# Performance work log

Measured on AMD Instinct MI355X. Metric: run time of the kernel, lower is better.

Reference implementation:

```python
import jax, jax.numpy as jnp
import numpy as np

SEQ_LEN, BATCH, INPUT_SIZE, HIDDEN_SIZE = 2048, 512, 64, 128


def setup_inputs() -> dict:
    key = jax.random.key(0)
    kx, k1, kb1, k2, kb2 = jax.random.split(key, 5)
    s1 = 1.0 / np.sqrt(INPUT_SIZE)
    s2 = 1.0 / np.sqrt(HIDDEN_SIZE)
    return {
        "x": jax.random.normal(kx, (SEQ_LEN, BATCH, INPUT_SIZE), dtype=jnp.float32),
        "W1": jax.random.uniform(k1, (HIDDEN_SIZE, INPUT_SIZE), jnp.float32, -s1, s1),
        "b1": jax.random.uniform(kb1, (HIDDEN_SIZE,), jnp.float32, -s1, s1),
        "W2": jax.random.uniform(k2, (HIDDEN_SIZE, HIDDEN_SIZE), jnp.float32, -s2, s2),
        "b2": jax.random.uniform(kb2, (HIDDEN_SIZE,), jnp.float32, -s2, s2),
    }


def reference(x, W1, b1, W2, b2):
    # Elman RNN: h_t = tanh(fc2(h_{t-1}) + fc1(x_t)), h_0 = 0
    # x: (S, B, I); W1: (H, I); W2: (H, H)
    B = x.shape[1]
    H = W2.shape[0]
    h0 = jnp.zeros((B, H), dtype=x.dtype)

    def step(h, x_t):
        h_new = jnp.tanh(x_t @ W1.T + b1 + h @ W2.T + b2)
        return h_new, h_new

    h_last, h_seq = jax.lax.scan(step, h0, x)
    return h_seq, h_last[None]  # (S,B,H), (1,B,H)
```

## Files before the change

### kernel.cpp

```cpp
#include <hip/hip_runtime.h>
#include <math.h>


#define S_LEN 2048
#define B_SZ  512
#define I_SZ  64
#define H_SZ  128
#define BT    16
#define BLK   512
#define HROW  256
#define XROW  128

typedef short bf16x8 __attribute__((ext_vector_type(8)));
typedef float f32x4  __attribute__((ext_vector_type(4)));

#define MFMA(A, B, C) __builtin_amdgcn_mfma_f32_16x16x32_bf16((A), (B), (C), 0, 0, 0)

#define LDS_BARRIER()                                        \
    asm volatile("s_waitcnt lgkmcnt(0)" ::: "memory");       \
    __builtin_amdgcn_s_barrier();                            \
    asm volatile("" ::: "memory")

__device__ __forceinline__ unsigned short bf_trunc(float v) {
    union { float f; unsigned u; } x; x.f = v;
    return (unsigned short)(x.u >> 16);
}
__device__ __forceinline__ float bf_to_f(unsigned short h) {
    union { float f; unsigned u; } x; x.u = ((unsigned)h) << 16;
    return x.f;
}

__global__ __launch_bounds__(BLK) void rnn_mfma(
    const float* __restrict__ x,
    const float* __restrict__ W1,
    const float* __restrict__ b1,
    const float* __restrict__ W2,
    const float* __restrict__ b2,
    float* __restrict__ out)
{
    const int tid  = threadIdx.x;
    const int lane = tid & 63;
    const int w    = tid >> 6;
    const int l15  = lane & 15;
    const int l4   = lane >> 4;
    const int unit = (w << 4) + l15;
    const int b0   = blockIdx.x * BT;

    __shared__ short hpl_hi[2][BT * H_SZ];
    __shared__ short hpl_lo[2][BT * H_SZ];
    __shared__ short xpl_hi[2][BT * I_SZ];
    __shared__ short xpl_lo[2][BT * I_SZ];

    bf16x8 w2h[4], w2l[4], w1h[2], w1l[2];
    #pragma unroll
    for (int c = 0; c < 4; ++c) {
        #pragma unroll
        for (int j = 0; j < 8; ++j) {
            float v = W2[unit * H_SZ + 32 * c + l4 * 8 + j];
            unsigned short hi = bf_trunc(v);
            unsigned short lo = bf_trunc(v - bf_to_f(hi));
            w2h[c][j] = (short)hi; w2l[c][j] = (short)lo;
        }
    }
    #pragma unroll
    for (int c = 0; c < 2; ++c) {
        #pragma unroll
        for (int j = 0; j < 8; ++j) {
            float v = W1[unit * I_SZ + 32 * c + l4 * 8 + j];
            unsigned short hi = bf_trunc(v);
            unsigned short lo = bf_trunc(v - bf_to_f(hi));
            w1h[c][j] = (short)hi; w1l[c][j] = (short)lo;
        }
    }
    const float zb = b1[unit] + b2[unit];

    int hro[4], xro[2], woh[4];
    #pragma unroll
    for (int c = 0; c < 4; ++c)
        hro[c] = l15 * HROW + ((64 * c + l4 * 16) ^ ((l15 & 7) << 4));
    #pragma unroll
    for (int c = 0; c < 2; ++c)
        xro[c] = l15 * XROW + ((64 * c + l4 * 16) ^ ((l15 & 7) << 4));
    #pragma unroll
    for (int r = 0; r < 4; ++r) {
        int row = (l4 << 2) + r;
        woh[r] = row * HROW + ((unit * 2) ^ ((row & 7) << 4));
    }
    const int xr  = tid >> 5;
    const int xc  = (tid & 31) * 2;
    const int wox = xr * XROW + ((xc * 2) ^ ((xr & 7) << 4));

    {
        float2 v0 = *(const float2*)(x + ((size_t)0 * B_SZ + b0 + xr) * I_SZ + xc);
        unsigned short h0 = bf_trunc(v0.x), h1 = bf_trunc(v0.y);
        unsigned short g0 = bf_trunc(v0.x - bf_to_f(h0));
        unsigned short g1 = bf_trunc(v0.y - bf_to_f(h1));
        *(unsigned*)((char*)xpl_hi[0] + wox) = (unsigned)h0 | ((unsigned)h1 << 16);
        *(unsigned*)((char*)xpl_lo[0] + wox) = (unsigned)g0 | ((unsigned)g1 << 16);
    }
    float2 xgA = *(const float2*)(x + ((size_t)1 * B_SZ + b0 + xr) * I_SZ + xc);
    float2 xgB;

    LDS_BARRIER();

    bf16x8 ah[4], al[4], xh[2], xl[2];
    #pragma unroll
    for (int c = 0; c < 4; ++c) { ah[c] = (bf16x8){0,0,0,0,0,0,0,0}; al[c] = ah[c]; }
    #pragma unroll
    for (int c = 0; c < 2; ++c) {
        xh[c] = *(const bf16x8*)((const char*)xpl_hi[0] + xro[c]);
        xl[c] = *(const bf16x8*)((const char*)xpl_lo[0] + xro[c]);
    }

#define STEP(S, XGC, XGL, HB)                                                 \
{                                                                             \
                 \
    { int sp = (S) + 2; if (sp > S_LEN - 1) sp = S_LEN - 1;                   \
      XGL = *(const float2*)(x + ((size_t)sp * B_SZ + b0 + xr) * I_SZ + xc); }\
    f32x4 accA = {zb, zb, zb, zb};                                            \
    f32x4 accB = {0.f, 0.f, 0.f, 0.f};                                       \
    f32x4 accC = {0.f, 0.f, 0.f, 0.f};                                       \
    accA = MFMA(ah[0], w2h[0], accA);  accB = MFMA(al[0], w2h[0], accB);      \
    accC = MFMA(ah[0], w2l[0], accC);                                         \
    accA = MFMA(ah[1], w2h[1], accA);  accB = MFMA(al[1], w2h[1], accB);      \
    accC = MFMA(ah[1], w2l[1], accC);                                         \
    accA = MFMA(ah[2], w2h[2], accA);  accB = MFMA(al[2], w2h[2], accB);      \
    accC = MFMA(ah[2], w2l[2], accC);                                         \
    accA = MFMA(ah[3], w2h[3], accA);  accB = MFMA(al[3], w2h[3], accB);      \
    accC = MFMA(ah[3], w2l[3], accC);                                         \
    accA = MFMA(xh[0], w1h[0], accA);  accB = MFMA(xl[0], w1h[0], accB);      \
    accC = MFMA(xh[0], w1l[0], accC);                                         \
    accA = MFMA(xh[1], w1h[1], accA);  accB = MFMA(xl[1], w1h[1], accB);      \
    accC = MFMA(xh[1], w1l[1], accC);                                         \
    f32x4 acc = (accA + accB) + accC;                                         \
                      \
    _Pragma("unroll")                                                         \
    for (int r = 0; r < 4; ++r) {                                             \
        float a = acc[r];                                                     \
        float t = 1.0f - 2.0f * __builtin_amdgcn_rcpf(1.0f + __expf(2.0f*a)); \
        int row = (l4 << 2) + r;                                              \
        out[((size_t)(S) * B_SZ + b0 + row) * H_SZ + unit] = t;               \
        unsigned short hi = bf_trunc(t);                                      \
        unsigned short lo = bf_trunc(t - bf_to_f(hi));                        \
        *(short*)((char*)hpl_hi[HB] + woh[r]) = (short)hi;                    \
        *(short*)((char*)hpl_lo[HB] + woh[r]) = (short)lo;                    \
    }                                                                         \
                        \
    {                                                                         \
        unsigned short h0 = bf_trunc(XGC.x), h1 = bf_trunc(XGC.y);            \
        unsigned short g0 = bf_trunc(XGC.x - bf_to_f(h0));                    \
        unsigned short g1 = bf_trunc(XGC.y - bf_to_f(h1));                    \
        *(unsigned*)((char*)xpl_hi[HB] + wox) = (unsigned)h0|((unsigned)h1<<16);\
        *(unsigned*)((char*)xpl_lo[HB] + wox) = (unsigned)g0|((unsigned)g1<<16);\
    }                                                                         \
    LDS_BARRIER();                                                            \
                                                \
    _Pragma("unroll")                                                         \
    for (int c = 0; c < 4; ++c) {                                             \
        ah[c] = *(const bf16x8*)((const char*)hpl_hi[HB] + hro[c]);           \
        al[c] = *(const bf16x8*)((const char*)hpl_lo[HB] + hro[c]);           \
    }                                                                         \
    _Pragma("unroll")                                                         \
    for (int c = 0; c < 2; ++c) {                                             \
        xh[c] = *(const bf16x8*)((const char*)xpl_hi[HB] + xro[c]);           \
        xl[c] = *(const bf16x8*)((const char*)xpl_lo[HB] + xro[c]);           \
    }                                                                         \
}

    for (int s2 = 0; s2 < S_LEN; s2 += 2) {
        STEP(s2,     xgA, xgB, 1);
        STEP(s2 + 1, xgB, xgA, 0);
    }
#undef STEP

    #pragma unroll
    for (int r = 0; r < 4; ++r) {
        int row = (l4 << 2) + r;
        unsigned short hi = (unsigned short)*(short*)((char*)hpl_hi[0] + woh[r]);
        unsigned short lo = (unsigned short)*(short*)((char*)hpl_lo[0] + woh[r]);
        float hv = bf_to_f(hi) + bf_to_f(lo);
        out[(size_t)S_LEN * B_SZ * H_SZ + (size_t)(b0 + row) * H_SZ + unit] = hv;
    }
}

extern "C" void kernel_launch(void* const* d_in, const int* in_sizes, int n_in,
                              void* d_out, int out_size, void* d_ws, size_t ws_size,
                              hipStream_t stream) {
    const float* x  = (const float*)d_in[0];
    const float* W1 = (const float*)d_in[1];
    const float* b1 = (const float*)d_in[2];
    const float* W2 = (const float*)d_in[3];
    const float* b2 = (const float*)d_in[4];
    float* out = (float*)d_out;

    rnn_mfma<<<dim3(B_SZ / BT), dim3(BLK), 0, stream>>>(x, W1, b1, W2, b2, out);
}
```

Before: 1.297 ms.

## Hoist input projection into parallel prepass and shrink recurrent block to two waves

Splits the work into a fully parallel prepass that computes x·W1ᵀ+b1+b2 for all timesteps into the output buffer, and a recurrent kernel that only does the h·W2ᵀ MFMAs. The recurrent block drops from 8 waves to 2, with each wave handling 64 hidden units, and the hidden state is stored as fp32 in LDS and split into hi/lo on read. This takes the input MFMAs and x conversion off the serial critical path and means fewer waves per barrier. The cost is an extra full-size write and read of the precomputed terms, and the final h_last is now the fp32 value rather than the hi+lo sum.

New measurement: 2.879 ms. 122% more time.

```diff
diff --git a/kernel.cpp b/kernel.cpp
--- a/kernel.cpp
+++ b/kernel.cpp
@@ -7,9 +7,10 @@
 #define I_SZ  64
 #define H_SZ  128
 #define BT    16
-#define BLK   512
-#define HROW  256
-#define XROW  128
+#define NTILE 32
+#define BLK1  512
+#define BLK2  128
+#define SBH   (B_SZ * H_SZ)
 
 typedef short bf16x8 __attribute__((ext_vector_type(8)));
 typedef float f32x4  __attribute__((ext_vector_type(4)));
@@ -21,21 +22,73 @@
     __builtin_amdgcn_s_barrier();                            \
     asm volatile("" ::: "memory")
 
+__device__ __forceinline__ unsigned fbits(float v) {
+    union { float f; unsigned u; } x; x.f = v; return x.u;
+}
+__device__ __forceinline__ float fval(unsigned u) {
+    union { float f; unsigned u; } x; x.u = u; return x.f;
+}
+__device__ __forceinline__ unsigned short bf_rnd(float v) {
+    return (unsigned short)((fbits(v) + 0x8000u) >> 16);
+}
 __device__ __forceinline__ unsigned short bf_trunc(float v) {
-    union { float f; unsigned u; } x; x.f = v;
-    return (unsigned short)(x.u >> 16);
-}
-__device__ __forceinline__ float bf_to_f(unsigned short h) {
-    union { float f; unsigned u; } x; x.u = ((unsigned)h) << 16;
-    return x.f;
-}
-
-__global__ __launch_bounds__(BLK) void rnn_mfma(
+    return (unsigned short)(fbits(v) >> 16);
+}
+__device__ __forceinline__ void split8t(float4 a, float4 b, bf16x8* hi, bf16x8* lo) {
+    float v[8] = {a.x, a.y, a.z, a.w, b.x, b.y, b.z, b.w};
+    #pragma unroll
+    for (int j = 0; j < 8; ++j) {
+        unsigned short h = bf_trunc(v[j]);
+        (*hi)[j] = (short)h;
+        (*lo)[j] = (short)bf_trunc(v[j] - fval(((unsigned)h) << 16));
+    }
+}
+
+__global__ __launch_bounds__(BLK1) void rnn_prepass(
     const float* __restrict__ x,
     const float* __restrict__ W1,
     const float* __restrict__ b1,
+    const float* __restrict__ b2,
+    float* __restrict__ z)
+{
+    const int tid  = threadIdx.x;
+    const int lane = tid & 63;
+    const int w    = tid >> 6;
+    const int l15  = lane & 15;
+    const int l4   = lane >> 4;
+    const int unit = (w << 4) + l15;
+    const int bid  = blockIdx.x;
+    const int s    = bid >> 5;
+    const int b0   = (bid & 31) << 4;
+
+    bf16x8 w1h[2], w1l[2];
+    #pragma unroll
+    for (int c = 0; c < 2; ++c) {
+        const float* wr = W1 + unit * I_SZ + 32 * c + l4 * 8;
+        split8t(*(const float4*)wr, *(const float4*)(wr + 4), &w1h[c], &w1l[c]);
+    }
+    const float zb = b1[unit] + b2[unit];
+
+    bf16x8 xh[2], xl[2];
+    const float* xr = x + ((size_t)s * B_SZ + b0 + l15) * I_SZ + l4 * 8;
+    #pragma unroll
+    for (int c = 0; c < 2; ++c)
+        split8t(*(const float4*)(xr + 32 * c), *(const float4*)(xr + 32 * c + 4),
+                &xh[c], &xl[c]);
+
+    f32x4 acc  = {zb, zb, zb, zb};
+    f32x4 acc2 = {0.f, 0.f, 0.f, 0.f};
+    acc  = MFMA(xh[0], w1h[0], acc);   acc  = MFMA(xh[1], w1h[1], acc);
+    acc2 = MFMA(xl[0], w1h[0], acc2);  acc2 = MFMA(xl[1], w1h[1], acc2);
+    acc2 = MFMA(xh[0], w1l[0], acc2);  acc2 = MFMA(xh[1], w1l[1], acc2);
+    acc += acc2;
+
+    *(f32x4*)(z + ((size_t)bid * 8 + w) * 256 + lane * 4) = acc;
+}
+
+__global__ __launch_bounds__(BLK2, 1) void rnn_recur(
     const float* __restrict__ W2,
-    const float* __restrict__ b2,
+    const float* __restrict__ zr,
     float* __restrict__ out)
 {
     const int tid  = threadIdx.x;
@@ -43,143 +96,129 @@
     const int w    = tid >> 6;
     const int l15  = lane & 15;
     const int l4   = lane >> 4;
-    const int unit = (w << 4) + l15;
-    const int b0   = blockIdx.x * BT;
-
-    __shared__ short hpl_hi[2][BT * H_SZ];
-    __shared__ short hpl_lo[2][BT * H_SZ];
-    __shared__ short xpl_hi[2][BT * I_SZ];
-    __shared__ short xpl_lo[2][BT * I_SZ];
-
-    bf16x8 w2h[4], w2l[4], w1h[2], w1l[2];
-    #pragma unroll
-    for (int c = 0; c < 4; ++c) {
-        #pragma unroll
-        for (int j = 0; j < 8; ++j) {
-            float v = W2[unit * H_SZ + 32 * c + l4 * 8 + j];
-            unsigned short hi = bf_trunc(v);
-            unsigned short lo = bf_trunc(v - bf_to_f(hi));
-            w2h[c][j] = (short)hi; w2l[c][j] = (short)lo;
+    const int tile = blockIdx.x;
+    const int b0   = tile << 4;
+
+    __shared__ float hplane[2][BT * H_SZ];
+
+    bf16x8 w2h[4][4], w2l[4][4];
+    #pragma unroll
+    for (int t = 0; t < 4; ++t) {
+        const int n = (w << 6) + (t << 4) + l15;
+        #pragma unroll
+        for (int c = 0; c < 4; ++c) {
+            const float* wr = W2 + n * H_SZ + 32 * c + l4 * 8;
+            split8t(*(const float4*)wr, *(const float4*)(wr + 4),
+                    &w2h[t][c], &w2l[t][c]);
         }
     }
-    #pragma unroll
-    for (int c = 0; c < 2; ++c) {
-        #pragma unroll
-        for (int j = 0; j < 8; ++j) {
-            float v = W1[unit * I_SZ + 32 * c + l4 * 8 + j];
-            unsigned short hi = bf_trunc(v);
-            unsigned short lo = bf_trunc(v - bf_to_f(hi));
-            w1h[c][j] = (short)hi; w1l[c][j] = (short)lo;
+
+    int rb[4][2];
+    #pragma unroll
+    for (int c = 0; c < 4; ++c)
+        #pragma unroll
+        for (int hh = 0; hh < 2; ++hh)
+            rb[c][hh] = l15 * 512 +
+                ((((32 * c + l4 * 8 + 4 * hh) << 2)) ^ ((l15 & 7) << 4));
+    int wb[4][4];
+    #pragma unroll
+    for (int t = 0; t < 4; ++t)
+        #pragma unroll
+        for (int r = 0; r < 4; ++r) {
+            int row = (l4 << 2) + r;
+            wb[t][r] = row * 512 +
+                ((((w << 6) + (t << 4) + l15) << 2) ^ ((row & 7) << 4));
         }
-    }
-    const float zb = b1[unit] + b2[unit];
-
-    int hro[4], xro[2], woh[4];
-    #pragma unroll
-    for (int c = 0; c < 4; ++c)
-        hro[c] = l15 * HROW + ((64 * c + l4 * 16) ^ ((l15 & 7) << 4));
-    #pragma unroll
-    for (int c = 0; c < 2; ++c)
-        xro[c] = l15 * XROW + ((64 * c + l4 * 16) ^ ((l15 & 7) << 4));
-    #pragma unroll
-    for (int r = 0; r < 4; ++r) {
-        int row = (l4 << 2) + r;
-        woh[r] = row * HROW + ((unit * 2) ^ ((row & 7) << 4));
-    }
-    const int xr  = tid >> 5;
-    const int xc  = (tid & 31) * 2;
-    const int wox = xr * XROW + ((xc * 2) ^ ((xr & 7) << 4));
+
+    const float* zp = zr + (size_t)tile * 2048 + (size_t)(4 * w) * 256 + lane * 4;
+    const size_t obase = (size_t)(b0 + (l4 << 2)) * H_SZ + (w << 6) + l15;
+
+    f32x4 zA[4], zB[4];
+    #pragma unroll
+    for (int t = 0; t < 4; ++t) {
+        zA[t] = *(const f32x4*)(zp + t * 256);
+        zB[t] = *(const f32x4*)(zp + t * 256 + SBH);
+    }
+    bf16x8 ah[4], al[4];
+    #pragma unroll
+    for (int c = 0; c < 4; ++c) { ah[c] = (bf16x8){0,0,0,0,0,0,0,0}; al[c] = ah[c]; }
+    float tl[4][4];
+    union U { unsigned u[4]; bf16x8 v; };
+
+#define BODY(S, P, ZQ)                                                        \
+{                                                                             \
+    f32x4 acc[4], a2[4], a3[4];                                               \
+    _Pragma("unroll")                                                         \
+    for (int t = 0; t < 4; ++t) {                                             \
+        acc[t] = ZQ[t];                                                       \
+        a2[t] = (f32x4){0.f,0.f,0.f,0.f};  a3[t] = a2[t];                     \
+    }                                                                         \
+                   \
+    { int sp = (S) + 2; if (sp > S_LEN - 1) sp = S_LEN - 1;                   \
+      const float* zs = zp + (size_t)sp * SBH;                                \
+      _Pragma("unroll")                                                       \
+      for (int t = 0; t < 4; ++t) ZQ[t] = *(const f32x4*)(zs + t * 256); }    \
+    _Pragma("unroll")                                                         \
+    for (int c = 0; c < 4; ++c) {                                             \
+        _Pragma("unroll")                                                     \
+        for (int t = 0; t < 4; ++t) {                                         \
+            acc[t] = MFMA(ah[c], w2h[t][c], acc[t]);                          \
+            a2[t]  = MFMA(al[c], w2h[t][c], a2[t]);                           \
+            a3[t]  = MFMA(ah[c], w2l[t][c], a3[t]);                           \
+        }                                                                     \
+    }                                                                         \
+    float* po = out + (size_t)(S) * SBH + obase;                              \
+    _Pragma("unroll")                                                         \
+    for (int t = 0; t < 4; ++t) {                                             \
+        _Pragma("unroll")                                                     \
+        for (int r = 0; r < 4; ++r) {                                         \
+            float a = (acc[t][r] + a2[t][r]) + a3[t][r];                      \
+            float tt = 1.0f - 2.0f * __builtin_amdgcn_rcpf(1.0f + __expf(2.0f*a)); \
+            tl[t][r] = tt;                                                    \
+            po[(size_t)r * H_SZ + t * 16] = tt;                               \
+            *(float*)((char*)hplane[P] + wb[t][r]) = tt;                      \
+        }                                                                     \
+    }                                                                         \
+    LDS_BARRIER();                                                            \
+              \
+    _Pragma("unroll")                                                         \
+    for (int c = 0; c < 4; ++c) {                                             \
+        uint4 d0 = *(const uint4*)((const char*)hplane[P] + rb[c][0]);        \
+        uint4 d1 = *(const uint4*)((const char*)hplane[P] + rb[c][1]);        \
+        U uh, ul;                                                             \
+        uh.u[0] = __builtin_amdgcn_perm(d0.y, d0.x, 0x07060302u);             \
+        uh.u[1] = __builtin_amdgcn_perm(d0.w, d0.z, 0x07060302u);             \
+        uh.u[2] = __builtin_amdgcn_perm(d1.y, d1.x, 0x07060302u);             \
+        uh.u[3] = __builtin_amdgcn_perm(d1.w, d1.z, 0x07060302u);             \
+        unsigned e0 = fbits(fval(d0.x) - fval(d0.x & 0xffff0000u));           \
+        unsigned e1 = fbits(fval(d0.y) - fval(d0.y & 0xffff0000u));           \
+        unsigned e2 = fbits(fval(d0.z) - fval(d0.z & 0xffff0000u));           \
+        unsigned e3 = fbits(fval(d0.w) - fval(d0.w & 0xffff0000u));           \
+        unsigned e4 = fbits(fval(d1.x) - fval(d1.x & 0xffff0000u));           \
+        unsigned e5 = fbits(fval(d1.y) - fval(d1.y & 0xffff0000u));           \
+        unsigned e6 = fbits(fval(d1.z) - fval(d1.z & 0xffff0000u));           \
+        unsigned e7 = fbits(fval(d1.w) - fval(d1.w & 0xffff0000u));           \
+        ul.u[0] = __builtin_amdgcn_perm(e1, e0, 0x07060302u);                 \
+        ul.u[1] = __builtin_amdgcn_perm(e3, e2, 0x07060302u);                 \
+        ul.u[2] = __builtin_amdgcn_perm(e5, e4, 0x07060302u);                 \
+        ul.u[3] = __builtin_amdgcn_perm(e7, e6, 0x07060302u);                 \
+        ah[c] = uh.v;  al[c] = ul.v;                                          \
+    }                                                                         \
+}
+
+    for (int s2 = 0; s2 < S_LEN; s2 += 2) {
+        BODY(s2,     0, zA);
+        BODY(s2 + 1, 1, zB);
+    }
+#undef BODY
 
     {
-        float2 v0 = *(const float2*)(x + ((size_t)0 * B_SZ + b0 + xr) * I_SZ + xc);
-        unsigned short h0 = bf_trunc(v0.x), h1 = bf_trunc(v0.y);
-        unsigned short g0 = bf_trunc(v0.x - bf_to_f(h0));
-        unsigned short g1 = bf_trunc(v0.y - bf_to_f(h1));
-        *(unsigned*)((char*)xpl_hi[0] + wox) = (unsigned)h0 | ((unsigned)h1 << 16);
-        *(unsigned*)((char*)xpl_lo[0] + wox) = (unsigned)g0 | ((unsigned)g1 << 16);
-    }
-    float2 xgA = *(const float2*)(x + ((size_t)1 * B_SZ + b0 + xr) * I_SZ + xc);
-    float2 xgB;
-
-    LDS_BARRIER();
-
-    bf16x8 ah[4], al[4], xh[2], xl[2];
-    #pragma unroll
-    for (int c = 0; c < 4; ++c) { ah[c] = (bf16x8){0,0,0,0,0,0,0,0}; al[c] = ah[c]; }
-    #pragma unroll
-    for (int c = 0; c < 2; ++c) {
-        xh[c] = *(const bf16x8*)((const char*)xpl_hi[0] + xro[c]);
-        xl[c] = *(const bf16x8*)((const char*)xpl_lo[0] + xro[c]);
-    }
-
-#define STEP(S, XGC, XGL, HB)                                                 \
-{                                                                             \
-                 \
-    { int sp = (S) + 2; if (sp > S_LEN - 1) sp = S_LEN - 1;                   \
-      XGL = *(const float2*)(x + ((size_t)sp * B_SZ + b0 + xr) * I_SZ + xc); }\
-    f32x4 accA = {zb, zb, zb, zb};                                            \
-    f32x4 accB = {0.f, 0.f, 0.f, 0.f};                                       \
-    f32x4 accC = {0.f, 0.f, 0.f, 0.f};                                       \
-    accA = MFMA(ah[0], w2h[0], accA);  accB = MFMA(al[0], w2h[0], accB);      \
-    accC = MFMA(ah[0], w2l[0], accC);                                         \
-    accA = MFMA(ah[1], w2h[1], accA);  accB = MFMA(al[1], w2h[1], accB);      \
-    accC = MFMA(ah[1], w2l[1], accC);                                         \
-    accA = MFMA(ah[2], w2h[2], accA);  accB = MFMA(al[2], w2h[2], accB);      \
-    accC = MFMA(ah[2], w2l[2], accC);                                         \
-    accA = MFMA(ah[3], w2h[3], accA);  accB = MFMA(al[3], w2h[3], accB);      \
-    accC = MFMA(ah[3], w2l[3], accC);                                         \
-    accA = MFMA(xh[0], w1h[0], accA);  accB = MFMA(xl[0], w1h[0], accB);      \
-    accC = MFMA(xh[0], w1l[0], accC);                                         \
-    accA = MFMA(xh[1], w1h[1], accA);  accB = MFMA(xl[1], w1h[1], accB);      \
-    accC = MFMA(xh[1], w1l[1], accC);                                         \
-    f32x4 acc = (accA + accB) + accC;                                         \
-                      \
-    _Pragma("unroll")                                                         \
-    for (int r = 0; r < 4; ++r) {                                             \
-        float a = acc[r];                                                     \
-        float t = 1.0f - 2.0f * __builtin_amdgcn_rcpf(1.0f + __expf(2.0f*a)); \
-        int row = (l4 << 2) + r;                                              \
-        out[((size_t)(S) * B_SZ + b0 + row) * H_SZ + unit] = t;               \
-        unsigned short hi = bf_trunc(t);                                      \
-        unsigned short lo = bf_trunc(t - bf_to_f(hi));                        \
-        *(short*)((char*)hpl_hi[HB] + woh[r]) = (short)hi;                    \
-        *(short*)((char*)hpl_lo[HB] + woh[r]) = (short)lo;                    \
-    }                                                                         \
-                        \
-    {                                                                         \
-        unsigned short h0 = bf_trunc(XGC.x), h1 = bf_trunc(XGC.y);            \
-        unsigned short g0 = bf_trunc(XGC.x - bf_to_f(h0));                    \
-        unsigned short g1 = bf_trunc(XGC.y - bf_to_f(h1));                    \
-        *(unsigned*)((char*)xpl_hi[HB] + wox) = (unsigned)h0|((unsigned)h1<<16);\
-        *(unsigned*)((char*)xpl_lo[HB] + wox) = (unsigned)g0|((unsigned)g1<<16);\
-    }                                                                         \
-    LDS_BARRIER();                                                            \
-                                                \
-    _Pragma("unroll")                                                         \
-    for (int c = 0; c < 4; ++c) {                                             \
-        ah[c] = *(const bf16x8*)((const char*)hpl_hi[HB] + hro[c]);           \
-        al[c] = *(const bf16x8*)((const char*)hpl_lo[HB] + hro[c]);           \
-    }                                                                         \
-    _Pragma("unroll")                                                         \
-    for (int c = 0; c < 2; ++c) {                                             \
-        xh[c] = *(const bf16x8*)((const char*)xpl_hi[HB] + xro[c]);           \
-        xl[c] = *(const bf16x8*)((const char*)xpl_lo[HB] + xro[c]);           \
-    }                                                                         \
-}
-
-    for (int s2 = 0; s2 < S_LEN; s2 += 2) {
-        STEP(s2,     xgA, xgB, 1);
-        STEP(s2 + 1, xgB, xgA, 0);
-    }
-#undef STEP
-
-    #pragma unroll
-    for (int r = 0; r < 4; ++r) {
-        int row = (l4 << 2) + r;
-        unsigned short hi = (unsigned short)*(short*)((char*)hpl_hi[0] + woh[r]);
-        unsigned short lo = (unsigned short)*(short*)((char*)hpl_lo[0] + woh[r]);
-        float hv = bf_to_f(hi) + bf_to_f(lo);
-        out[(size_t)S_LEN * B_SZ * H_SZ + (size_t)(b0 + row) * H_SZ + unit] = hv;
+        float* po = out + (size_t)S_LEN * SBH + obase;
+        #pragma unroll
+        for (int t = 0; t < 4; ++t)
+            #pragma unroll
+            for (int r = 0; r < 4; ++r)
+                po[(size_t)r * H_SZ + t * 16] = tl[t][r];
     }
 }
 
@@ -193,5 +232,6 @@
     const float* b2 = (const float*)d_in[4];
     float* out = (float*)d_out;
 
-    rnn_mfma<<<dim3(B_SZ / BT), dim3(BLK), 0, stream>>>(x, W1, b1, W2, b2, out);
-}
+    rnn_prepass<<<dim3(S_LEN * NTILE), dim3(BLK1), 0, stream>>>(x, W1, b1, b2, out);
+    rnn_recur<<<dim3(NTILE), dim3(BLK2), 0, stream>>>(W2, out, out);
+}
```
